# Kernel optimization log

Hardware: AMD Instinct MI355X
Metric: run time of the kernel (lower is better)

## Reference

```python
import jax, jax.numpy as jnp
import numpy as np


def kernel_mus(n_kernels):
    l_mu = [1.0]
    if n_kernels == 1:
        return l_mu
    bin_size = 2.0 / (n_kernels - 1)
    l_mu.append(1 - bin_size / 2)
    for i in range(1, n_kernels - 1):
        l_mu.append(l_mu[i] - bin_size)
    return l_mu


def kernel_sigmas(n_kernels):
    bin_size = 2.0 / (n_kernels - 1)
    l_sigma = [0.0001]
    if n_kernels == 1:
        return l_sigma
    l_sigma += [0.5 * bin_size] * (n_kernels - 1)
    return l_sigma


def setup_inputs() -> dict:
    key = jax.random.key(0)
    k0, k1, k2, k3 = jax.random.split(key, 4)
    B, Q, D, E, V, K = 256, 32, 512, 300, 100000, 11
    query_tokens = jax.random.randint(k0, (B, Q), 0, V)
    doc_tokens = jax.random.randint(k1, (B, D), 0, V)
    emb_table = jax.random.normal(k2, (V, E), jnp.float32) * 0.02
    dense_w = jax.random.uniform(k3, (1, K), jnp.float32, -0.014, 0.014)
    dense_b = jnp.zeros((1,), jnp.float32)
    mu = jnp.asarray(kernel_mus(K), jnp.float32)
    sigma = jnp.asarray(kernel_sigmas(K), jnp.float32)
    return {"query_tokens": query_tokens, "doc_tokens": doc_tokens,
            "emb_table": emb_table, "dense_w": dense_w, "dense_b": dense_b,
            "mu": mu, "sigma": sigma}


def reference(query_tokens, doc_tokens, emb_table, dense_w, dense_b, mu, sigma):
    EPS = 1e-13  # CosineMatrixAttention tiny value
    q_mask = (query_tokens > 0).astype(jnp.float32)   # [B,Q]
    d_mask = (doc_tokens > 0).astype(jnp.float32)     # [B,D]
    q_emb = emb_table[query_tokens]                   # [B,Q,E]
    d_emb = emb_table[doc_tokens]                     # [B,D,E]
    q_n = q_emb / (jnp.linalg.norm(q_emb, axis=-1, keepdims=True) + EPS)
    d_n = d_emb / (jnp.linalg.norm(d_emb, axis=-1, keepdims=True) + EPS)
    cosine = jnp.einsum('bqe,bde->bqd', q_n, d_n)     # [B,Q,D]
    pair_mask = q_mask[:, :, None] * d_mask[:, None, :]  # [B,Q,D]
    cosine_masked = cosine * pair_mask
    # gaussian kernels: [B,Q,D,K]
    diff = cosine_masked[..., None] - mu
    kernels = jnp.exp(-(diff * diff) / (2.0 * sigma * sigma)) * pair_mask[..., None]
    per_kernel_query = jnp.sum(kernels, axis=2)       # [B,Q,K]
    log_pkq = jnp.log(jnp.clip(per_kernel_query, 1e-10)) * 0.01
    log_pkq = log_pkq * q_mask[..., None]
    per_kernel = jnp.sum(log_pkq, axis=1)             # [B,K]
    out = per_kernel @ dense_w.T + dense_b            # [B,1]
    return out[:, 0]
```

## Files before the change

### kernel.cpp

```cpp
#include <hip/hip_runtime.h>


#define B      256
#define BQ     32
#define BD     512
#define EDIM   300
#define KPAD   320
#define NK     11
#define NSEMI  32
#define QSTR   328

typedef float floatx4 __attribute__((ext_vector_type(4)));
typedef short shortx8 __attribute__((ext_vector_type(8)));

__device__ __forceinline__ unsigned short f2bf(float f) {
    unsigned int u = __float_as_uint(f);
    return (unsigned short)((u + 0x7fffu + ((u >> 16) & 1u)) >> 16);
}
__device__ __forceinline__ float bf2f(unsigned short h) {
    return __uint_as_float(((unsigned int)h) << 16);
}
__device__ __forceinline__ float sbc(float x) {
    return __uint_as_float(__builtin_amdgcn_readfirstlane(__float_as_uint(x)));
}

__global__ __launch_bounds__(256)
void knrm_norm(const float* __restrict__ emb, unsigned short* __restrict__ ebf,
               float* __restrict__ rnorm, int V)
{
    int r    = blockIdx.x * 16 + (threadIdx.x >> 4);
    int part = threadIdx.x & 15;
    if (r >= V) return;
    const float4* src = (const float4*)(emb + (size_t)r * EDIM);
    uint2*        dst = (uint2*)(ebf + (size_t)r * KPAD);
    float ss = 0.f;
    #pragma unroll
    for (int i = 0; i < 5; ++i) {
        int c = part + i * 16;
        uint2 p = {0u, 0u};
        if (c < EDIM / 4) {
            float4 v = src[c];
            unsigned short h0 = f2bf(v.x), h1 = f2bf(v.y), h2 = f2bf(v.z), h3 = f2bf(v.w);
            p.x = (unsigned int)h0 | ((unsigned int)h1 << 16);
            p.y = (unsigned int)h2 | ((unsigned int)h3 << 16);
            float f0 = bf2f(h0), f1 = bf2f(h1), f2 = bf2f(h2), f3 = bf2f(h3);
            ss += f0 * f0 + f1 * f1 + f2 * f2 + f3 * f3;
        }
        dst[c] = p;
    }
    ss += __shfl_xor(ss, 1);
    ss += __shfl_xor(ss, 2);
    ss += __shfl_xor(ss, 4);
    ss += __shfl_xor(ss, 8);
    if (part == 0) rnorm[r] = 1.f / (sqrtf(ss) + 1e-13f);
}

__global__ __launch_bounds__(256, 5)
void knrm_main5(const int* __restrict__ qtok, const int* __restrict__ dtok,
                const unsigned short* __restrict__ ebf, const float* __restrict__ rnorm,
                const float* __restrict__ mu, const float* __restrict__ sigma,
                float* __restrict__ pkq_part)
{
    __shared__ unsigned short q_buf[BQ * QSTR];
    __shared__ float rqs[BQ];

    const int tid  = threadIdx.x;
    const int lane = tid & 63;
    const int wv   = tid >> 6;
    const int b    = blockIdx.x & 255;
    const int g    = blockIdx.x >> 8;
    const int l16  = lane & 15;
    const int quad = lane >> 4;

    const int td = dtok[b * BD + g * 64 + wv * 16 + l16];
    const float rd = rnorm[td];
    const float dm = (td > 0) ? 1.f : 0.f;

    const uint4* bsrc = (const uint4*)(ebf + (size_t)td * KPAD);
    shortx8 bfrag[10];
    #pragma unroll
    for (int ks = 0; ks < 10; ++ks)
        bfrag[ks] = *(const shortx8*)&bsrc[quad + ks * 4];

    if (tid < BQ) rqs[tid] = rnorm[qtok[b * BQ + tid]];

    {
        int row = tid >> 3, part = tid & 7;
        int tok = qtok[b * BQ + row];
        const uint4* src = (const uint4*)(ebf + (size_t)tok * KPAD);
        #pragma unroll
        for (int i = 0; i < 5; ++i) {
            int c = part + i * 8;
            *(uint4*)&q_buf[row * QSTR + c * 8] = src[c];
        }
    }
    __syncthreads();

    float mur[NK], cfr[NK];
    #pragma unroll
    for (int k = 0; k < NK; ++k) {
        float s = sbc(sigma[k]);
        mur[k] = sbc(mu[k]);
        cfr[k] = -0.5f / (s * s);
    }

    const unsigned short* a0 = &q_buf[l16 * QSTR + quad * 8];
    const unsigned short* a1 = a0 + 16 * QSTR;

    floatx4 acc0 = {0.f, 0.f, 0.f, 0.f};
    floatx4 acc1 = {0.f, 0.f, 0.f, 0.f};
    #pragma unroll
    for (int ks = 0; ks < 10; ++ks) {
        shortx8 aA = *(const shortx8*)(a0 + ks * 32);
        shortx8 aB = *(const shortx8*)(a1 + ks * 32);
        acc0 = __builtin_amdgcn_mfma_f32_16x16x32_bf16(aA, bfrag[ks], acc0, 0, 0, 0);
        acc1 = __builtin_amdgcn_mfma_f32_16x16x32_bf16(aB, bfrag[ks], acc1, 0, 0, 0);
    }

    const int semi = g * 4 + wv;
    float* dst = pkq_part + (size_t)(b * NSEMI + semi) * (BQ * NK);

    #pragma unroll
    for (int slab = 0; slab < 2; ++slab) {
        floatx4 acc = slab ? acc1 : acc0;
        #pragma unroll
        for (int r = 0; r < 4; ++r) {
            int q = slab * 16 + quad * 4 + r;
            float c0 = acc[r] * rqs[q] * rd;
            #pragma unroll
            for (int k = 0; k < NK; ++k) {
                float d0 = c0 - mur[k];
                float v = dm * __expf(cfr[k] * d0 * d0);
                v += __shfl_xor(v, 1);
                v += __shfl_xor(v, 2);
                v += __shfl_xor(v, 4);
                v += __shfl_xor(v, 8);
                if (l16 == 0) dst[q * NK + k] = v;
            }
        }
    }
}

__global__ __launch_bounds__(64)
void knrm_epi(const int* __restrict__ qtok, const float* __restrict__ dw,
              const float* __restrict__ db, const float* __restrict__ pkq_part,
              float* __restrict__ out)
{
    int b = blockIdx.x, lane = threadIdx.x;
    float sq = 0.f;
    if (lane < BQ) {
        int tok = qtok[b * BQ + lane];
        if (tok > 0) {
            #pragma unroll
            for (int k = 0; k < NK; ++k) {
                float s = 0.f;
                #pragma unroll
                for (int c = 0; c < NSEMI; ++c)
                    s += pkq_part[((size_t)(b * NSEMI + c) * BQ + lane) * NK + k];
                sq += __logf(fmaxf(s, 1e-10f)) * 0.01f * dw[k];
            }
        }
    }
    sq += __shfl_xor(sq, 1);
    sq += __shfl_xor(sq, 2);
    sq += __shfl_xor(sq, 4);
    sq += __shfl_xor(sq, 8);
    sq += __shfl_xor(sq, 16);
    sq += __shfl_xor(sq, 32);
    if (lane == 0) out[b] = sq + db[0];
}

extern "C" void kernel_launch(void* const* d_in, const int* in_sizes, int n_in,
                              void* d_out, int out_size, void* d_ws, size_t ws_size,
                              hipStream_t stream)
{
    const int*   qtok  = (const int*)d_in[0];
    const int*   dtok  = (const int*)d_in[1];
    const float* emb   = (const float*)d_in[2];
    const float* dw    = (const float*)d_in[3];
    const float* dbias = (const float*)d_in[4];
    const float* mu    = (const float*)d_in[5];
    const float* sg    = (const float*)d_in[6];
    float* out = (float*)d_out;

    const int V = in_sizes[2] / EDIM;
    const size_t ebf_bytes = (size_t)V * KPAD * 2;
    const size_t rn_bytes  = (size_t)V * 4;

    unsigned short* ebf = (unsigned short*)d_ws;
    float* rnorm        = (float*)((char*)d_ws + ebf_bytes);
    float* pkq_part     = (float*)((char*)d_ws + ebf_bytes + rn_bytes);

    knrm_norm<<<(V + 15) / 16, 256, 0, stream>>>(emb, ebf, rnorm, V);
    knrm_main5<<<B * 8, 256, 0, stream>>>(qtok, dtok, ebf, rnorm, mu, sg, pkq_part);
    knrm_epi<<<B, 64, 0, stream>>>(qtok, dw, dbias, pkq_part, out);
}
```

Before: 248.5 us.

## Process four doc slabs per wave with register accumulation and LDS reduction

Each block now covers half of a batch row's documents, with every wave looping over four 16-doc slabs. The next slab's embedding fragments are double-buffered, and Gaussian kernel sums accumulate in registers across slabs. Cross-lane shuffles run once per accumulated value instead of once per slab, and partials are combined in shared memory with atomics, so only two partials per batch go to global memory. The epilogue therefore reads 2 partials instead of 32. Register use rises and there are fewer, larger blocks, which may lower occupancy and parallelism.

```diff
diff --git a/kernel.cpp b/kernel.cpp
--- a/kernel.cpp
+++ b/kernel.cpp
@@ -7,7 +7,6 @@
 #define EDIM   300
 #define KPAD   320
 #define NK     11
-#define NSEMI  32
 #define QSTR   328
 
 typedef float floatx4 __attribute__((ext_vector_type(4)));
@@ -55,34 +54,45 @@
     if (part == 0) rnorm[r] = 1.f / (sqrtf(ss) + 1e-13f);
 }
 
-__global__ __launch_bounds__(256, 5)
-void knrm_main5(const int* __restrict__ qtok, const int* __restrict__ dtok,
+__device__ __forceinline__ void load_frags(shortx8* bf, const unsigned short* __restrict__ ebf,
+                                           int tok, int quad)
+{
+    const uint4* src = (const uint4*)(ebf + (size_t)tok * KPAD);
+    #pragma unroll
+    for (int ks = 0; ks < 10; ++ks)
+        bf[ks] = *(const shortx8*)&src[quad + ks * 4];
+}
+
+__global__ __launch_bounds__(256)
+void knrm_main6(const int* __restrict__ qtok, const int* __restrict__ dtok,
                 const unsigned short* __restrict__ ebf, const float* __restrict__ rnorm,
                 const float* __restrict__ mu, const float* __restrict__ sigma,
                 float* __restrict__ pkq_part)
 {
     __shared__ unsigned short q_buf[BQ * QSTR];
+    __shared__ float pkq_s[BQ * NK];
     __shared__ float rqs[BQ];
 
     const int tid  = threadIdx.x;
     const int lane = tid & 63;
     const int wv   = tid >> 6;
     const int b    = blockIdx.x & 255;
-    const int g    = blockIdx.x >> 8;
+    const int half = blockIdx.x >> 8;
     const int l16  = lane & 15;
     const int quad = lane >> 4;
 
-    const int td = dtok[b * BD + g * 64 + wv * 16 + l16];
-    const float rd = rnorm[td];
-    const float dm = (td > 0) ? 1.f : 0.f;
-
-    const uint4* bsrc = (const uint4*)(ebf + (size_t)td * KPAD);
-    shortx8 bfrag[10];
-    #pragma unroll
-    for (int ks = 0; ks < 10; ++ks)
-        bfrag[ks] = *(const shortx8*)&bsrc[quad + ks * 4];
-
+    for (int i = tid; i < BQ * NK; i += 256) pkq_s[i] = 0.f;
     if (tid < BQ) rqs[tid] = rnorm[qtok[b * BQ + tid]];
+
+    const int dbase = b * BD + half * 256 + wv * 16 + l16;
+    int   td[4];
+    float rd[4], dm[4];
+    #pragma unroll
+    for (int s = 0; s < 4; ++s) {
+        td[s] = dtok[dbase + s * 64];
+        rd[s] = rnorm[td[s]];
+        dm[s] = (td[s] > 0) ? 1.f : 0.f;
+    }
 
     {
         int row = tid >> 3, part = tid & 7;
@@ -94,6 +104,10 @@
             *(uint4*)&q_buf[row * QSTR + c * 8] = src[c];
         }
     }
+
+    shortx8 bf0[10], bf1[10];
+    load_frags(bf0, ebf, td[0], quad);
+
     __syncthreads();
 
     float mur[NK], cfr[NK];
@@ -103,42 +117,73 @@
         mur[k] = sbc(mu[k]);
         cfr[k] = -0.5f / (s * s);
     }
+    float rqv[8];
+    #pragma unroll
+    for (int slab = 0; slab < 2; ++slab)
+        #pragma unroll
+        for (int r = 0; r < 4; ++r)
+            rqv[slab * 4 + r] = rqs[slab * 16 + quad * 4 + r];
 
     const unsigned short* a0 = &q_buf[l16 * QSTR + quad * 8];
     const unsigned short* a1 = a0 + 16 * QSTR;
 
-    floatx4 acc0 = {0.f, 0.f, 0.f, 0.f};
-    floatx4 acc1 = {0.f, 0.f, 0.f, 0.f};
-    #pragma unroll
-    for (int ks = 0; ks < 10; ++ks) {
-        shortx8 aA = *(const shortx8*)(a0 + ks * 32);
-        shortx8 aB = *(const shortx8*)(a1 + ks * 32);
-        acc0 = __builtin_amdgcn_mfma_f32_16x16x32_bf16(aA, bfrag[ks], acc0, 0, 0, 0);
-        acc1 = __builtin_amdgcn_mfma_f32_16x16x32_bf16(aB, bfrag[ks], acc1, 0, 0, 0);
-    }
-
-    const int semi = g * 4 + wv;
-    float* dst = pkq_part + (size_t)(b * NSEMI + semi) * (BQ * NK);
-
-    #pragma unroll
-    for (int slab = 0; slab < 2; ++slab) {
-        floatx4 acc = slab ? acc1 : acc0;
-        #pragma unroll
-        for (int r = 0; r < 4; ++r) {
-            int q = slab * 16 + quad * 4 + r;
-            float c0 = acc[r] * rqs[q] * rd;
+    float pk[2][4][NK];
+    #pragma unroll
+    for (int slab = 0; slab < 2; ++slab)
+        #pragma unroll
+        for (int r = 0; r < 4; ++r)
+            #pragma unroll
+            for (int k = 0; k < NK; ++k) pk[slab][r][k] = 0.f;
+
+    #pragma unroll
+    for (int s = 0; s < 4; ++s) {
+        const shortx8* bf = (s & 1) ? bf1 : bf0;
+
+        floatx4 acc0 = {0.f, 0.f, 0.f, 0.f};
+        floatx4 acc1 = {0.f, 0.f, 0.f, 0.f};
+        #pragma unroll
+        for (int ks = 0; ks < 10; ++ks) {
+            shortx8 aA = *(const shortx8*)(a0 + ks * 32);
+            shortx8 aB = *(const shortx8*)(a1 + ks * 32);
+            acc0 = __builtin_amdgcn_mfma_f32_16x16x32_bf16(aA, bf[ks], acc0, 0, 0, 0);
+            acc1 = __builtin_amdgcn_mfma_f32_16x16x32_bf16(aB, bf[ks], acc1, 0, 0, 0);
+        }
+
+        if (s < 3) load_frags((s & 1) ? bf0 : bf1, ebf, td[s + 1], quad);
+
+        #pragma unroll
+        for (int slab = 0; slab < 2; ++slab) {
+            floatx4 acc = slab ? acc1 : acc0;
+            #pragma unroll
+            for (int r = 0; r < 4; ++r) {
+                float c0 = acc[r] * rqv[slab * 4 + r] * rd[s];
+                #pragma unroll
+                for (int k = 0; k < NK; ++k) {
+                    float d0 = c0 - mur[k];
+                    pk[slab][r][k] += dm[s] * __expf(cfr[k] * d0 * d0);
+                }
+            }
+        }
+    }
+
+    #pragma unroll
+    for (int slab = 0; slab < 2; ++slab)
+        #pragma unroll
+        for (int r = 0; r < 4; ++r)
             #pragma unroll
             for (int k = 0; k < NK; ++k) {
-                float d0 = c0 - mur[k];
-                float v = dm * __expf(cfr[k] * d0 * d0);
+                float v = pk[slab][r][k];
                 v += __shfl_xor(v, 1);
                 v += __shfl_xor(v, 2);
                 v += __shfl_xor(v, 4);
                 v += __shfl_xor(v, 8);
-                if (l16 == 0) dst[q * NK + k] = v;
+                if (l16 == 0)
+                    atomicAdd(&pkq_s[(slab * 16 + quad * 4 + r) * NK + k], v);
             }
-        }
-    }
+    __syncthreads();
+
+    float* dst = pkq_part + (size_t)(b * 2 + half) * (BQ * NK);
+    for (int i = tid; i < BQ * NK; i += 256) dst[i] = pkq_s[i];
 }
 
 __global__ __launch_bounds__(64)
@@ -153,10 +198,8 @@
         if (tok > 0) {
             #pragma unroll
             for (int k = 0; k < NK; ++k) {
-                float s = 0.f;
-                #pragma unroll
-                for (int c = 0; c < NSEMI; ++c)
-                    s += pkq_part[((size_t)(b * NSEMI + c) * BQ + lane) * NK + k];
+                float s = pkq_part[((size_t)(b * 2 + 0) * BQ + lane) * NK + k]
+                        + pkq_part[((size_t)(b * 2 + 1) * BQ + lane) * NK + k];
                 sq += __logf(fmaxf(s, 1e-10f)) * 0.01f * dw[k];
             }
         }
@@ -192,6 +235,6 @@
     float* pkq_part     = (float*)((char*)d_ws + ebf_bytes + rn_bytes);
 
     knrm_norm<<<(V + 15) / 16, 256, 0, stream>>>(emb, ebf, rnorm, V);
-    knrm_main5<<<B * 8, 256, 0, stream>>>(qtok, dtok, ebf, rnorm, mu, sg, pkq_part);
+    knrm_main6<<<B * 2, 256, 0, stream>>>(qtok, dtok, ebf, rnorm, mu, sg, pkq_part);
     knrm_epi<<<B, 64, 0, stream>>>(qtok, dw, dbias, pkq_part, out);
 }
```

After: 231.4 us. 6.9% less time.
